# Kernel tuning notes

Measured on AMD Instinct MI355X. Metric: run time of the kernel, lower is better.

The kernel has to match this reference:

```python
import jax, jax.numpy as jnp
import numpy as np

EPS = 1e-5  # torch BatchNorm1d default

def _batchnorm(x, gamma, beta):
    # Training-mode BatchNorm1d: biased variance over the batch dim.
    mean = jnp.mean(x, axis=0)
    var = jnp.mean(jnp.square(x - mean), axis=0)
    return (x - mean) * jax.lax.rsqrt(var + EPS) * gamma + beta

def setup_inputs() -> dict:
    key = jax.random.key(0)
    ks = jax.random.split(key, 8)
    N, nfeat, nhid, nclass = 32768, 2048, 4096, 512
    x = jax.random.normal(ks[0], (N, nfeat), dtype=jnp.float32)
    y = jax.random.normal(ks[1], (N, nclass), dtype=jnp.float32)
    # Linear params (kaiming-uniform-ish scale)
    W1 = jax.random.uniform(ks[2], (nhid, nfeat), jnp.float32, -1.0, 1.0) / np.sqrt(nfeat)
    b1 = jax.random.uniform(ks[3], (nhid,), jnp.float32, -1.0, 1.0) / np.sqrt(nfeat)
    W2 = jax.random.uniform(ks[4], (nclass, nhid), jnp.float32, -1.0, 1.0) / np.sqrt(nhid)
    b2 = jax.random.uniform(ks[5], (nclass,), jnp.float32, -1.0, 1.0) / np.sqrt(nhid)
    # BatchNorm affine params (torch init: gamma=1, beta=0)
    bn1_g = jnp.ones((nfeat,), jnp.float32)
    bn1_b = jnp.zeros((nfeat,), jnp.float32)
    bn2_g = jnp.ones((nhid,), jnp.float32)
    bn2_b = jnp.zeros((nhid,), jnp.float32)
    # InteractionUnit: single learnable interaction strength beta
    beta = jnp.array(0.5, jnp.float32)
    return {"x": x, "y": y, "W1": W1, "b1": b1, "W2": W2, "b2": b2,
            "bn1_g": bn1_g, "bn1_b": bn1_b, "bn2_g": bn2_g, "bn2_b": bn2_b,
            "beta": beta}

def reference(x, y, W1, b1, W2, b2, bn1_g, bn1_b, bn2_g, bn2_b, beta):
    h = _batchnorm(x, bn1_g, bn1_b)                 # [N, nfeat]
    h = jax.nn.relu(h @ W1.T + b1)                  # [N, nhid]
    h = _batchnorm(h, bn2_g, bn2_b)                 # [N, nhid]
    out = h @ W2.T + b2 + beta * y                  # [N, nclass]
    return out
```

## Files before the change

### kernel.cpp

```cpp
#include <hip/hip_runtime.h>

typedef __bf16 v8bf __attribute__((ext_vector_type(8)));
typedef float  v16f __attribute__((ext_vector_type(16)));
typedef float  f4   __attribute__((ext_vector_type(4)));
typedef unsigned int uint;
typedef unsigned short ushort;
typedef uint   v4u  __attribute__((ext_vector_type(4)));
typedef uint   v2u  __attribute__((ext_vector_type(2)));

#define GLAS(p) ((const __attribute__((address_space(1))) void*)(p))
#define LDAS(p) ((__attribute__((address_space(3))) void*)(p))

__device__ __forceinline__ ushort f32_to_bf16(float f) {
    uint u = __builtin_bit_cast(uint, f);
    uint r = u + 0x7FFFu + ((u >> 16) & 1u);
    return (ushort)(r >> 16);
}
__device__ __forceinline__ float bflo(uint v) { return __builtin_bit_cast(float, v << 16); }
__device__ __forceinline__ float bfhi(uint v) { return __builtin_bit_cast(float, v & 0xFFFF0000u); }

__global__ void colstats_cvt(const float* __restrict__ x, ushort* __restrict__ xb,
                             float* __restrict__ sum, float* __restrict__ ssum,
                             int ncols, int rows) {
    int c4 = blockIdx.x * blockDim.x + threadIdx.x;
    int q = ncols >> 2;
    size_t base = (size_t)blockIdx.y * rows * q + c4;
    const f4* x4 = (const f4*)x;
    v2u* o = (v2u*)xb;
    f4 s = {0.f, 0.f, 0.f, 0.f}, qq = {0.f, 0.f, 0.f, 0.f};
#pragma unroll 4
    for (int r = 0; r < rows; ++r) {
        f4 v = x4[base + (size_t)r * q];
        s += v; qq += v * v;
        union { ushort us[4]; v2u u; } p;
        p.us[0] = f32_to_bf16(v.x); p.us[1] = f32_to_bf16(v.y);
        p.us[2] = f32_to_bf16(v.z); p.us[3] = f32_to_bf16(v.w);
        o[base + (size_t)r * q] = p.u;
    }
    atomicAdd(&sum[4 * c4 + 0], s.x);  atomicAdd(&ssum[4 * c4 + 0], qq.x);
    atomicAdd(&sum[4 * c4 + 1], s.y);  atomicAdd(&ssum[4 * c4 + 1], qq.y);
    atomicAdd(&sum[4 * c4 + 2], s.z);  atomicAdd(&ssum[4 * c4 + 2], qq.z);
    atomicAdd(&sum[4 * c4 + 3], s.w);  atomicAdd(&ssum[4 * c4 + 3], qq.w);
}

__global__ void colstats_bf16(const ushort* __restrict__ h, float* __restrict__ sum,
                              float* __restrict__ ssum, int ncols, int rows) {
    int cp = blockIdx.x * blockDim.x + threadIdx.x;
    int half = ncols >> 1;
    const uint* h32 = (const uint*)h;
    size_t base = (size_t)blockIdx.y * rows * half + cp;
    float s0 = 0.f, q0 = 0.f, s1 = 0.f, q1 = 0.f;
#pragma unroll 4
    for (int r = 0; r < rows; ++r) {
        uint v = h32[base + (size_t)r * half];
        float a = bflo(v), b = bfhi(v);
        s0 += a; q0 += a * a;
        s1 += b; q1 += b * b;
    }
    atomicAdd(&sum[2 * cp], s0);  atomicAdd(&ssum[2 * cp], q0);
    atomicAdd(&sum[2 * cp + 1], s1); atomicAdd(&ssum[2 * cp + 1], q1);
}

__global__ void bn_finalize(const float* __restrict__ sum, const float* __restrict__ ssum,
                            const float* __restrict__ g, const float* __restrict__ b,
                            float* __restrict__ s, float* __restrict__ t, float invN) {
    int c = blockIdx.x * blockDim.x + threadIdx.x;
    float m = sum[c] * invN;
    float var = fmaxf(ssum[c] * invN - m * m, 0.f);
    float rs = rsqrtf(var + 1e-5f);
    float sc = rs * g[c];
    s[c] = sc;
    t[c] = b[c] - m * sc;
}

__global__ void fold_w(const float* __restrict__ W, const float* __restrict__ bias,
                       const float* __restrict__ s, const float* __restrict__ t,
                       ushort* __restrict__ Wp, float* __restrict__ bp, int K) {
    int j = blockIdx.x, tx = threadIdx.x;
    const f4* row = (const f4*)(W + (size_t)j * K);
    const f4* s4 = (const f4*)s;
    const f4* t4 = (const f4*)t;
    v2u* orow = (v2u*)(Wp + (size_t)j * K);
    float part = 0.f;
    int K4 = K >> 2;
    for (int k = tx; k < K4; k += 256) {
        f4 v = row[k], sv = s4[k], tv = t4[k];
        part += v.x * tv.x + v.y * tv.y + v.z * tv.z + v.w * tv.w;
        union { ushort us[4]; v2u u; } o;
        o.us[0] = f32_to_bf16(v.x * sv.x);
        o.us[1] = f32_to_bf16(v.y * sv.y);
        o.us[2] = f32_to_bf16(v.z * sv.z);
        o.us[3] = f32_to_bf16(v.w * sv.w);
        orow[k] = o.u;
    }
    __shared__ float red[256];
    red[tx] = part;
    __syncthreads();
    for (int off = 128; off > 0; off >>= 1) {
        if (tx < off) red[tx] += red[tx + off];
        __syncthreads();
    }
    if (tx == 0) bp[j] = bias[j] + red[0];
}

template <int EPI>
__global__ __launch_bounds__(256) void gemm_bt(
    const ushort* __restrict__ A, const ushort* __restrict__ B,
    void* __restrict__ Cout, const float* __restrict__ bias,
    const float* __restrict__ Y, const float* __restrict__ betaPtr,
    int M, int Ncol, int K) {
    __shared__ __align__(16) ushort lsA[128 * 64];
    __shared__ __align__(16) ushort lsB[128 * 64];
    const int tid = threadIdx.x;
    const int wave = tid >> 6, lane = tid & 63;
    const int wm = wave >> 1, wn = wave & 1;
    const int l32 = lane & 31, lq = lane >> 5;
    const int m0 = blockIdx.y * 128, n0 = blockIdx.x * 128;

    const int srow = lane >> 3;
    const int sgc  = (lane & 7) ^ (lane >> 3);

    v16f acc[2][2] = {};

    for (int k0 = 0; k0 < K; k0 += 64) {
#pragma unroll
        for (int q = 0; q < 4; ++q) {
            const int g0 = (q * 4 + wave) << 6;
            const int row = (g0 >> 3) + srow;
            const ushort* sa = A + (size_t)(m0 + row) * K + k0 + sgc * 8;
            const ushort* sb = B + (size_t)(n0 + row) * K + k0 + sgc * 8;
            __builtin_amdgcn_global_load_lds(GLAS(sa), LDAS(&lsA[g0 * 8]), 16, 0, 0);
            __builtin_amdgcn_global_load_lds(GLAS(sb), LDAS(&lsB[g0 * 8]), 16, 0, 0);
        }
        __syncthreads();
#pragma unroll
        for (int kk = 0; kk < 64; kk += 16) {
            v8bf a[2], b[2];
            const int cbase = (kk >> 3) + lq;
#pragma unroll
            for (int i = 0; i < 2; ++i) {
                const int ra = wm * 64 + i * 32 + l32;
                const int pa = ra * 8 + (cbase ^ (ra & 7));
                a[i] = __builtin_bit_cast(v8bf, *(const v4u*)&lsA[pa * 8]);
            }
#pragma unroll
            for (int j = 0; j < 2; ++j) {
                const int rb = wn * 64 + j * 32 + l32;
                const int pb = rb * 8 + (cbase ^ (rb & 7));
                b[j] = __builtin_bit_cast(v8bf, *(const v4u*)&lsB[pb * 8]);
            }
#pragma unroll
            for (int i = 0; i < 2; ++i)
#pragma unroll
                for (int j = 0; j < 2; ++j)
                    acc[i][j] = __builtin_amdgcn_mfma_f32_32x32x16_bf16(a[i], b[j], acc[i][j], 0, 0, 0);
        }
        __syncthreads();
    }

    const float betaV = (EPI == 1) ? betaPtr[0] : 0.f;
#pragma unroll
    for (int j = 0; j < 2; ++j) {
        const int col = n0 + wn * 64 + j * 32 + l32;
        const float bj = bias[col];
#pragma unroll
        for (int i = 0; i < 2; ++i) {
#pragma unroll
            for (int reg = 0; reg < 16; ++reg) {
                const int row = m0 + wm * 64 + i * 32 + (reg & 3) + 8 * (reg >> 2) + 4 * lq;
                float v = acc[i][j][reg] + bj;
                if (EPI == 0) {
                    v = v > 0.f ? v : 0.f;
                    ((ushort*)Cout)[(size_t)row * Ncol + col] = f32_to_bf16(v);
                } else {
                    v += betaV * Y[(size_t)row * Ncol + col];
                    ((float*)Cout)[(size_t)row * Ncol + col] = v;
                }
            }
        }
    }
}

extern "C" void kernel_launch(void* const* d_in, const int* in_sizes, int n_in,
                              void* d_out, int out_size, void* d_ws, size_t ws_size,
                              hipStream_t stream) {
    const float* x    = (const float*)d_in[0];
    const float* y    = (const float*)d_in[1];
    const float* W1   = (const float*)d_in[2];
    const float* b1   = (const float*)d_in[3];
    const float* W2   = (const float*)d_in[4];
    const float* b2   = (const float*)d_in[5];
    const float* bn1g = (const float*)d_in[6];
    const float* bn1b = (const float*)d_in[7];
    const float* bn2g = (const float*)d_in[8];
    const float* bn2b = (const float*)d_in[9];
    const float* beta = (const float*)d_in[10];

    constexpr int Nb = 32768, F = 2048, H = 4096, C = 512;

    char* w = (char*)d_ws;
    ushort* xb  = (ushort*)w;
    ushort* h1  = (ushort*)(w + (size_t)Nb * F * 2);
    ushort* w1p = (ushort*)(w + (size_t)Nb * F * 2 + (size_t)Nb * H * 2);
    ushort* w2p = (ushort*)((char*)w1p + (size_t)H * F * 2);
    float*  fb  = (float*)((char*)w2p + (size_t)C * H * 2);
    float* b1p = fb;
    float* b2p = b1p + H;
    float* sum1 = b2p + C;
    float* ss1  = sum1 + F;
    float* s1   = ss1 + F;
    float* t1   = s1 + F;
    float* sum2 = t1 + F;
    float* ss2  = sum2 + H;
    float* s2   = ss2 + H;
    float* t2   = s2 + H;

    hipMemsetAsync(sum1, 0, sizeof(float) * 2 * F, stream);
    hipMemsetAsync(sum2, 0, sizeof(float) * 2 * H, stream);

    colstats_cvt<<<dim3(F / 4 / 256, 256), 256, 0, stream>>>(x, xb, sum1, ss1, F, Nb / 256);
    bn_finalize<<<F / 256, 256, 0, stream>>>(sum1, ss1, bn1g, bn1b, s1, t1, 1.f / Nb);
    fold_w<<<H, 256, 0, stream>>>(W1, b1, s1, t1, w1p, b1p, F);
    gemm_bt<0><<<dim3(H / 128, Nb / 128), 256, 0, stream>>>(xb, w1p, h1, b1p, nullptr, nullptr, Nb, H, F);
    colstats_bf16<<<dim3(H / 2 / 256, 128), 256, 0, stream>>>(h1, sum2, ss2, H, Nb / 128);
    bn_finalize<<<H / 256, 256, 0, stream>>>(sum2, ss2, bn2g, bn2b, s2, t2, 1.f / Nb);
    fold_w<<<C, 256, 0, stream>>>(W2, b2, s2, t2, w2p, b2p, H);
    gemm_bt<1><<<dim3(C / 128, Nb / 128), 256, 0, stream>>>(h1, w2p, d_out, b2p, y, beta, Nb, C, H);
    (void)in_sizes; (void)n_in; (void)out_size; (void)ws_size;
}
```

Measured before the change: 1.407 ms.

## Rewrite bf16 GEMM as 256x256 tile, 8-wave, double-buffered pipelined kernel

The GEMM goes from 128x128 tiles with 4 waves and a single LDS buffer to 256x256 tiles with 8 waves. It double-buffers LDS, staging half-tiles of the next k-slices during four compute phases, and uses explicit vmcnt/lgkmcnt waits, s_setprio and sched barriers. Workgroup IDs are remapped into an XCD-aware order for L2 locality. The aim is to raise arithmetic intensity and hide global-load latency behind MFMA work, at the cost of 128KB LDS per block, more registers and fragile hand-written wait counts.

```diff
diff --git a/kernel.cpp b/kernel.cpp
--- a/kernel.cpp
+++ b/kernel.cpp
@@ -103,72 +103,140 @@
     if (tx == 0) bp[j] = bias[j] + red[0];
 }
 
+
+__device__ __forceinline__ void stage_A(const ushort* __restrict__ Mat, ushort* dst,
+                                        int K, int k0, int ihalf, int wave, int lane) {
+    const int rs = lane >> 3;
+    const int gc = (lane & 7) ^ rs;
+    const int rb0 = ihalf * 64 + wave * 8;
+    const int rb1 = rb0 + 128;
+    const ushort* s0 = Mat + (size_t)(rb0 + rs) * K + k0 + gc * 8;
+    const ushort* s1 = Mat + (size_t)(rb1 + rs) * K + k0 + gc * 8;
+    __builtin_amdgcn_global_load_lds(GLAS(s0), LDAS(dst + rb0 * 64), 16, 0, 0);
+    __builtin_amdgcn_global_load_lds(GLAS(s1), LDAS(dst + rb1 * 64), 16, 0, 0);
+}
+__device__ __forceinline__ void stage_B(const ushort* __restrict__ Mat, ushort* dst,
+                                        int K, int k0, int jhalf, int wave, int lane) {
+    const int rs = lane >> 3;
+    const int gc = (lane & 7) ^ rs;
+    const int rb0 = (wave >> 2) * 64 + jhalf * 32 + (wave & 3) * 8;
+    const int rb1 = rb0 + 128;
+    const ushort* s0 = Mat + (size_t)(rb0 + rs) * K + k0 + gc * 8;
+    const ushort* s1 = Mat + (size_t)(rb1 + rs) * K + k0 + gc * 8;
+    __builtin_amdgcn_global_load_lds(GLAS(s0), LDAS(dst + rb0 * 64), 16, 0, 0);
+    __builtin_amdgcn_global_load_lds(GLAS(s1), LDAS(dst + rb1 * 64), 16, 0, 0);
+}
+
+#define PHASE(I, J, STAGE_STMT, WAIT_STMT)                                          \
+    {                                                                               \
+        v8bf a[2][4], b[4];                                                         \
+        _Pragma("unroll") for (int m2 = 0; m2 < 2; ++m2)                            \
+            _Pragma("unroll") for (int ks = 0; ks < 4; ++ks)                        \
+                a[m2][ks] = __builtin_bit_cast(                                     \
+                    v8bf, *(const v4u*)((const char*)curA + offA[I][m2][ks]));      \
+        _Pragma("unroll") for (int ks = 0; ks < 4; ++ks)                            \
+            b[ks] = __builtin_bit_cast(                                             \
+                v8bf, *(const v4u*)((const char*)curB + offB[J][ks]));              \
+        STAGE_STMT;                                                                 \
+        __builtin_amdgcn_s_barrier();                                               \
+        asm volatile("s_waitcnt lgkmcnt(0)" ::: "memory");                          \
+        __builtin_amdgcn_sched_barrier(0);                                          \
+        __builtin_amdgcn_s_setprio(1);                                              \
+        _Pragma("unroll") for (int ks = 0; ks < 4; ++ks)                            \
+            _Pragma("unroll") for (int m2 = 0; m2 < 2; ++m2)                        \
+                acc[I * 2 + m2][J] = __builtin_amdgcn_mfma_f32_32x32x16_bf16(       \
+                    a[m2][ks], b[ks], acc[I * 2 + m2][J], 0, 0, 0);                 \
+        __builtin_amdgcn_s_setprio(0);                                              \
+        __builtin_amdgcn_sched_barrier(0);                                          \
+        asm volatile("s_waitcnt lgkmcnt(0)" ::: "memory");                          \
+        WAIT_STMT;                                                                  \
+        __builtin_amdgcn_s_barrier();                                               \
+    }
+
 template <int EPI>
-__global__ __launch_bounds__(256) void gemm_bt(
+__global__ __launch_bounds__(512, 2) void gemm_bt(
     const ushort* __restrict__ A, const ushort* __restrict__ B,
     void* __restrict__ Cout, const float* __restrict__ bias,
     const float* __restrict__ Y, const float* __restrict__ betaPtr,
     int M, int Ncol, int K) {
-    __shared__ __align__(16) ushort lsA[128 * 64];
-    __shared__ __align__(16) ushort lsB[128 * 64];
+    __shared__ __align__(16) ushort lds[2][2][256 * 64];
     const int tid = threadIdx.x;
     const int wave = tid >> 6, lane = tid & 63;
-    const int wm = wave >> 1, wn = wave & 1;
-    const int l32 = lane & 31, lq = lane >> 5;
-    const int m0 = blockIdx.y * 128, n0 = blockIdx.x * 128;
-
-    const int srow = lane >> 3;
-    const int sgc  = (lane & 7) ^ (lane >> 3);
-
-    v16f acc[2][2] = {};
-
-    for (int k0 = 0; k0 < K; k0 += 64) {
-#pragma unroll
-        for (int q = 0; q < 4; ++q) {
-            const int g0 = (q * 4 + wave) << 6;
-            const int row = (g0 >> 3) + srow;
-            const ushort* sa = A + (size_t)(m0 + row) * K + k0 + sgc * 8;
-            const ushort* sb = B + (size_t)(n0 + row) * K + k0 + sgc * 8;
-            __builtin_amdgcn_global_load_lds(GLAS(sa), LDAS(&lsA[g0 * 8]), 16, 0, 0);
-            __builtin_amdgcn_global_load_lds(GLAS(sb), LDAS(&lsB[g0 * 8]), 16, 0, 0);
+    const int wm = wave >> 2, wn = wave & 3;
+    const int l31 = lane & 31, lq = lane >> 5;
+
+    const int gx = gridDim.x;
+    const int nwg = gx * gridDim.y;
+    int bid = blockIdx.y * gx + blockIdx.x;
+    const int qq = nwg >> 3;
+    bid = (bid & 7) * qq + (bid >> 3);
+    const int m0 = (bid / gx) * 256, n0 = (bid % gx) * 256;
+
+    const ushort* Ab = A + (size_t)m0 * K;
+    const ushort* Bb = B + (size_t)n0 * K;
+
+    int offA[2][2][4], offB[2][4];
+#pragma unroll
+    for (int I = 0; I < 2; ++I)
+#pragma unroll
+        for (int m2 = 0; m2 < 2; ++m2) {
+            const int rA = wm * 128 + I * 64 + m2 * 32 + l31;
+#pragma unroll
+            for (int ks = 0; ks < 4; ++ks)
+                offA[I][m2][ks] = (rA * 8 + ((ks * 2 + lq) ^ (rA & 7))) * 16;
         }
-        __syncthreads();
-#pragma unroll
-        for (int kk = 0; kk < 64; kk += 16) {
-            v8bf a[2], b[2];
-            const int cbase = (kk >> 3) + lq;
-#pragma unroll
-            for (int i = 0; i < 2; ++i) {
-                const int ra = wm * 64 + i * 32 + l32;
-                const int pa = ra * 8 + (cbase ^ (ra & 7));
-                a[i] = __builtin_bit_cast(v8bf, *(const v4u*)&lsA[pa * 8]);
-            }
-#pragma unroll
-            for (int j = 0; j < 2; ++j) {
-                const int rb = wn * 64 + j * 32 + l32;
-                const int pb = rb * 8 + (cbase ^ (rb & 7));
-                b[j] = __builtin_bit_cast(v8bf, *(const v4u*)&lsB[pb * 8]);
-            }
-#pragma unroll
-            for (int i = 0; i < 2; ++i)
-#pragma unroll
-                for (int j = 0; j < 2; ++j)
-                    acc[i][j] = __builtin_amdgcn_mfma_f32_32x32x16_bf16(a[i], b[j], acc[i][j], 0, 0, 0);
-        }
-        __syncthreads();
+#pragma unroll
+    for (int J = 0; J < 2; ++J) {
+        const int rB = wn * 64 + J * 32 + l31;
+#pragma unroll
+        for (int ks = 0; ks < 4; ++ks)
+            offB[J][ks] = (rB * 8 + ((ks * 2 + lq) ^ (rB & 7))) * 16;
+    }
+
+    v16f acc[4][2] = {};
+
+    const int NT = K >> 6;
+
+    stage_A(Ab, lds[0][0], K, 0, 0, wave, lane);
+    stage_B(Bb, lds[0][1], K, 0, 0, wave, lane);
+    stage_A(Ab, lds[0][0], K, 0, 1, wave, lane);
+    stage_B(Bb, lds[0][1], K, 0, 1, wave, lane);
+    if (NT > 1) {
+        stage_A(Ab, lds[1][0], K, 64, 0, wave, lane);
+        stage_B(Bb, lds[1][1], K, 64, 0, wave, lane);
+        asm volatile("s_waitcnt vmcnt(4)" ::: "memory");
+    } else {
+        asm volatile("s_waitcnt vmcnt(0)" ::: "memory");
+    }
+    __builtin_amdgcn_s_barrier();
+
+    for (int t = 0; t < NT; ++t) {
+        const int cb = t & 1, nb = cb ^ 1;
+        ushort* const curA = lds[cb][0];
+        ushort* const curB = lds[cb][1];
+        ushort* const nxtA = lds[nb][0];
+        ushort* const nxtB = lds[nb][1];
+        const int kN1 = (t + 1) << 6, kN2 = (t + 2) << 6;
+
+        PHASE(0, 0, if (t + 1 < NT) stage_A(Ab, nxtA, K, kN1, 1, wave, lane), )
+        PHASE(0, 1, if (t + 1 < NT) stage_B(Bb, nxtB, K, kN1, 1, wave, lane), )
+        PHASE(1, 0, if (t + 2 < NT) stage_A(Ab, curA, K, kN2, 0, wave, lane), )
+        PHASE(1, 1, if (t + 2 < NT) stage_B(Bb, curB, K, kN2, 0, wave, lane),
+              if (t + 2 < NT) { asm volatile("s_waitcnt vmcnt(4)" ::: "memory"); }
+              else { asm volatile("s_waitcnt vmcnt(0)" ::: "memory"); })
     }
 
     const float betaV = (EPI == 1) ? betaPtr[0] : 0.f;
 #pragma unroll
-    for (int j = 0; j < 2; ++j) {
-        const int col = n0 + wn * 64 + j * 32 + l32;
+    for (int nf = 0; nf < 2; ++nf) {
+        const int col = n0 + wn * 64 + nf * 32 + l31;
         const float bj = bias[col];
 #pragma unroll
-        for (int i = 0; i < 2; ++i) {
+        for (int mf = 0; mf < 4; ++mf) {
 #pragma unroll
             for (int reg = 0; reg < 16; ++reg) {
-                const int row = m0 + wm * 64 + i * 32 + (reg & 3) + 8 * (reg >> 2) + 4 * lq;
-                float v = acc[i][j][reg] + bj;
+                const int row = m0 + wm * 128 + mf * 32 + (reg & 3) + 8 * (reg >> 2) + 4 * lq;
+                float v = acc[mf][nf][reg] + bj;
                 if (EPI == 0) {
                     v = v > 0.f ? v : 0.f;
                     ((ushort*)Cout)[(size_t)row * Ncol + col] = f32_to_bf16(v);
@@ -179,6 +247,7 @@
             }
         }
     }
+    (void)M;
 }
 
 extern "C" void kernel_launch(void* const* d_in, const int* in_sizes, int n_in,
@@ -215,16 +284,16 @@
     float* s2   = ss2 + H;
     float* t2   = s2 + H;
 
-    hipMemsetAsync(sum1, 0, sizeof(float) * 2 * F, stream);
-    hipMemsetAsync(sum2, 0, sizeof(float) * 2 * H, stream);
+    (void)hipMemsetAsync(sum1, 0, sizeof(float) * 2 * F, stream);
+    (void)hipMemsetAsync(sum2, 0, sizeof(float) * 2 * H, stream);
 
     colstats_cvt<<<dim3(F / 4 / 256, 256), 256, 0, stream>>>(x, xb, sum1, ss1, F, Nb / 256);
     bn_finalize<<<F / 256, 256, 0, stream>>>(sum1, ss1, bn1g, bn1b, s1, t1, 1.f / Nb);
     fold_w<<<H, 256, 0, stream>>>(W1, b1, s1, t1, w1p, b1p, F);
-    gemm_bt<0><<<dim3(H / 128, Nb / 128), 256, 0, stream>>>(xb, w1p, h1, b1p, nullptr, nullptr, Nb, H, F);
+    gemm_bt<0><<<dim3(H / 256, Nb / 256), 512, 0, stream>>>(xb, w1p, h1, b1p, nullptr, nullptr, Nb, H, F);
     colstats_bf16<<<dim3(H / 2 / 256, 128), 256, 0, stream>>>(h1, sum2, ss2, H, Nb / 128);
     bn_finalize<<<H / 256, 256, 0, stream>>>(sum2, ss2, bn2g, bn2b, s2, t2, 1.f / Nb);
     fold_w<<<C, 256, 0, stream>>>(W2, b2, s2, t2, w2p, b2p, H);
-    gemm_bt<1><<<dim3(C / 128, Nb / 128), 256, 0, stream>>>(h1, w2p, d_out, b2p, y, beta, Nb, C, H);
+    gemm_bt<1><<<dim3(C / 256, Nb / 256), 512, 0, stream>>>(h1, w2p, d_out, b2p, y, beta, Nb, C, H);
     (void)in_sizes; (void)n_in; (void)out_size; (void)ws_size;
 }
```

Result: no change. 1.416 ms (+0.6%).

## Rewrite bf16 GEMM as 256x256 double-buffered pipelined kernel with 16x16 MFMA

Applied to the files above, without the earlier changes.

Replaces the 128x128 single-buffered GEMM with a 256x256-tile, 512-thread kernel. It splits each operand tile into halves held in a two-stage LDS ring and issues global-to-LDS loads for the next tiles between MFMA quadrants, using explicit vmcnt waits and barriers. It also switches to 16x16x32 MFMA with a new XOR swizzle, raises wave priority around the math, and remaps block IDs in an XCD-aware way for cache locality. The aim is to hide memory latency behind compute and improve data reuse. In exchange it needs much more LDS and registers, and the hand-managed sync makes correctness more fragile.

```diff
diff --git a/kernel.cpp b/kernel.cpp
--- a/kernel.cpp
+++ b/kernel.cpp
@@ -1,7 +1,6 @@
 #include <hip/hip_runtime.h>
 
 typedef __bf16 v8bf __attribute__((ext_vector_type(8)));
-typedef float  v16f __attribute__((ext_vector_type(16)));
 typedef float  f4   __attribute__((ext_vector_type(4)));
 typedef unsigned int uint;
 typedef unsigned short ushort;
@@ -103,72 +102,155 @@
     if (tx == 0) bp[j] = bias[j] + red[0];
 }
 
+
+__device__ __forceinline__ void stageA(const ushort* __restrict__ Mat, ushort* dstRegion,
+                                       int K, int k0, int I, int wave, int lane) {
+#pragma unroll
+    for (int h = 0; h < 2; ++h) {
+        const int rrb = h * 64 + wave * 8;
+        const int rr  = rrb + (lane >> 3);
+        const int cp  = (lane & 7) << 4;
+        const int gc  = cp ^ (((rr >> 2) & 1) << 5);
+        const int grow = (rr & 63) + ((rr >> 6) << 7) + I * 64;
+        const ushort* src = Mat + (size_t)grow * K + k0 + (gc >> 1);
+        __builtin_amdgcn_global_load_lds(GLAS(src), LDAS(dstRegion + rrb * 64), 16, 0, 0);
+    }
+}
+__device__ __forceinline__ void stageB(const ushort* __restrict__ Mat, ushort* dstRegion,
+                                       int K, int k0, int J, int wave, int lane) {
+#pragma unroll
+    for (int h = 0; h < 2; ++h) {
+        const int rrb = h * 64 + wave * 8;
+        const int rr  = rrb + (lane >> 3);
+        const int cp  = (lane & 7) << 4;
+        const int gc  = cp ^ (((rr >> 2) & 1) << 5);
+        const int gn  = (rr & 31) + ((rr >> 5) << 6) + J * 32;
+        const ushort* src = Mat + (size_t)gn * K + k0 + (gc >> 1);
+        __builtin_amdgcn_global_load_lds(GLAS(src), LDAS(dstRegion + rrb * 64), 16, 0, 0);
+    }
+}
+
+#define RD_A(rg)                                                                    \
+    _Pragma("unroll") for (int mf = 0; mf < 4; ++mf)                                \
+        _Pragma("unroll") for (int ks = 0; ks < 2; ++ks)                            \
+            a[mf][ks] = __builtin_bit_cast(                                         \
+                v8bf, *(const v4u*)((const char*)(rg) + offA[mf][ks]));
+
+#define RD_B(rg)                                                                    \
+    _Pragma("unroll") for (int nf = 0; nf < 2; ++nf)                                \
+        _Pragma("unroll") for (int ks = 0; ks < 2; ++ks)                            \
+            b[nf][ks] = __builtin_bit_cast(                                         \
+                v8bf, *(const v4u*)((const char*)(rg) + offB[nf][ks]));
+
+#define MM(I, J)                                                                    \
+    __builtin_amdgcn_s_barrier();                                                   \
+    __builtin_amdgcn_s_setprio(1);                                                  \
+    _Pragma("unroll") for (int ks = 0; ks < 2; ++ks)                                \
+        _Pragma("unroll") for (int mf = 0; mf < 4; ++mf)                            \
+            _Pragma("unroll") for (int nf = 0; nf < 2; ++nf)                        \
+                acc[(I) * 4 + mf][(J) * 2 + nf] =                                   \
+                    __builtin_amdgcn_mfma_f32_16x16x32_bf16(                        \
+                        a[mf][ks], b[nf][ks], acc[(I) * 4 + mf][(J) * 2 + nf],      \
+                        0, 0, 0);                                                   \
+    __builtin_amdgcn_s_setprio(0);
+
 template <int EPI>
-__global__ __launch_bounds__(256) void gemm_bt(
+__global__ __launch_bounds__(512, 2) void gemm_bt(
     const ushort* __restrict__ A, const ushort* __restrict__ B,
     void* __restrict__ Cout, const float* __restrict__ bias,
     const float* __restrict__ Y, const float* __restrict__ betaPtr,
     int M, int Ncol, int K) {
-    __shared__ __align__(16) ushort lsA[128 * 64];
-    __shared__ __align__(16) ushort lsB[128 * 64];
+    __shared__ __align__(16) ushort lds[2][4][128 * 64];
     const int tid = threadIdx.x;
     const int wave = tid >> 6, lane = tid & 63;
-    const int wm = wave >> 1, wn = wave & 1;
-    const int l32 = lane & 31, lq = lane >> 5;
-    const int m0 = blockIdx.y * 128, n0 = blockIdx.x * 128;
-
-    const int srow = lane >> 3;
-    const int sgc  = (lane & 7) ^ (lane >> 3);
-
-    v16f acc[2][2] = {};
-
-    for (int k0 = 0; k0 < K; k0 += 64) {
-#pragma unroll
-        for (int q = 0; q < 4; ++q) {
-            const int g0 = (q * 4 + wave) << 6;
-            const int row = (g0 >> 3) + srow;
-            const ushort* sa = A + (size_t)(m0 + row) * K + k0 + sgc * 8;
-            const ushort* sb = B + (size_t)(n0 + row) * K + k0 + sgc * 8;
-            __builtin_amdgcn_global_load_lds(GLAS(sa), LDAS(&lsA[g0 * 8]), 16, 0, 0);
-            __builtin_amdgcn_global_load_lds(GLAS(sb), LDAS(&lsB[g0 * 8]), 16, 0, 0);
-        }
-        __syncthreads();
-#pragma unroll
-        for (int kk = 0; kk < 64; kk += 16) {
-            v8bf a[2], b[2];
-            const int cbase = (kk >> 3) + lq;
-#pragma unroll
-            for (int i = 0; i < 2; ++i) {
-                const int ra = wm * 64 + i * 32 + l32;
-                const int pa = ra * 8 + (cbase ^ (ra & 7));
-                a[i] = __builtin_bit_cast(v8bf, *(const v4u*)&lsA[pa * 8]);
-            }
-#pragma unroll
-            for (int j = 0; j < 2; ++j) {
-                const int rb = wn * 64 + j * 32 + l32;
-                const int pb = rb * 8 + (cbase ^ (rb & 7));
-                b[j] = __builtin_bit_cast(v8bf, *(const v4u*)&lsB[pb * 8]);
-            }
-#pragma unroll
-            for (int i = 0; i < 2; ++i)
-#pragma unroll
-                for (int j = 0; j < 2; ++j)
-                    acc[i][j] = __builtin_amdgcn_mfma_f32_32x32x16_bf16(a[i], b[j], acc[i][j], 0, 0, 0);
-        }
-        __syncthreads();
+    const int wm = wave >> 2, wn = wave & 3;
+    const int l15 = lane & 15, l4 = lane >> 4;
+
+    const int gx = gridDim.x;
+    const int nwg = gx * gridDim.y;
+    int bid = blockIdx.y * gx + blockIdx.x;
+    const int qq = nwg >> 3;
+    bid = (bid & 7) * qq + (bid >> 3);
+    const int m0 = (bid / gx) * 256, n0 = (bid % gx) * 256;
+
+    const ushort* Ab = A + (size_t)m0 * K;
+    const ushort* Bb = B + (size_t)n0 * K;
+
+    int offA[4][2], offB[2][2];
+#pragma unroll
+    for (int mf = 0; mf < 4; ++mf) {
+        const int rr = wm * 64 + mf * 16 + l15;
+        const int sw = ((rr >> 2) & 1) << 5;
+#pragma unroll
+        for (int ks = 0; ks < 2; ++ks)
+            offA[mf][ks] = rr * 128 + ((ks * 64 + l4 * 16) ^ sw);
+    }
+#pragma unroll
+    for (int nf = 0; nf < 2; ++nf) {
+        const int rr = wn * 32 + nf * 16 + l15;
+        const int sw = ((rr >> 2) & 1) << 5;
+#pragma unroll
+        for (int ks = 0; ks < 2; ++ks)
+            offB[nf][ks] = rr * 128 + ((ks * 64 + l4 * 16) ^ sw);
+    }
+
+    f4 acc[8][4] = {};
+    v8bf a[4][2], b[2][2];
+
+    const int NT = K >> 6;
+
+    stageA(Ab, lds[0][0], K, 0, 0, wave, lane);
+    stageA(Ab, lds[0][1], K, 0, 1, wave, lane);
+    stageB(Bb, lds[0][2], K, 0, 0, wave, lane);
+    stageB(Bb, lds[0][3], K, 0, 1, wave, lane);
+    if (NT > 1) {
+        stageA(Ab, lds[1][0], K, 64, 0, wave, lane);
+        stageB(Bb, lds[1][3], K, 64, 1, wave, lane);
+        asm volatile("s_waitcnt vmcnt(4)" ::: "memory");
+    } else {
+        asm volatile("s_waitcnt vmcnt(0)" ::: "memory");
+    }
+    __builtin_amdgcn_s_barrier();
+
+    for (int t = 0; t < NT; ++t) {
+        const int cb = t & 1, nb = cb ^ 1;
+        const int kN1 = (t + 1) << 6, kN2 = (t + 2) << 6;
+
+        RD_A(lds[cb][0]);
+        RD_B(lds[cb][2]);
+        if (t + 1 < NT) stageA(Ab, lds[nb][1], K, kN1, 1, wave, lane);
+        MM(0, 0);
+        __builtin_amdgcn_s_barrier();
+
+        RD_B(lds[cb][3]);
+        if (t + 1 < NT) stageB(Bb, lds[nb][2], K, kN1, 0, wave, lane);
+        MM(0, 1);
+        __builtin_amdgcn_s_barrier();
+
+        RD_A(lds[cb][1]);
+        if (t + 2 < NT) stageA(Ab, lds[cb][0], K, kN2, 0, wave, lane);
+        MM(1, 1);
+        __builtin_amdgcn_s_barrier();
+
+        RD_B(lds[cb][2]);
+        if (t + 2 < NT) stageB(Bb, lds[cb][3], K, kN2, 1, wave, lane);
+        MM(1, 0);
+        if (t + 2 < NT) { asm volatile("s_waitcnt vmcnt(4)" ::: "memory"); }
+        else            { asm volatile("s_waitcnt vmcnt(0)" ::: "memory"); }
+        __builtin_amdgcn_s_barrier();
     }
 
     const float betaV = (EPI == 1) ? betaPtr[0] : 0.f;
 #pragma unroll
-    for (int j = 0; j < 2; ++j) {
-        const int col = n0 + wn * 64 + j * 32 + l32;
+    for (int Nf = 0; Nf < 4; ++Nf) {
+        const int col = n0 + wn * 64 + Nf * 16 + l15;
         const float bj = bias[col];
 #pragma unroll
-        for (int i = 0; i < 2; ++i) {
-#pragma unroll
-            for (int reg = 0; reg < 16; ++reg) {
-                const int row = m0 + wm * 64 + i * 32 + (reg & 3) + 8 * (reg >> 2) + 4 * lq;
-                float v = acc[i][j][reg] + bj;
+        for (int Mf = 0; Mf < 8; ++Mf) {
+#pragma unroll
+            for (int reg = 0; reg < 4; ++reg) {
+                const int row = m0 + wm * 128 + Mf * 16 + l4 * 4 + reg;
+                float v = acc[Mf][Nf][reg] + bj;
                 if (EPI == 0) {
                     v = v > 0.f ? v : 0.f;
                     ((ushort*)Cout)[(size_t)row * Ncol + col] = f32_to_bf16(v);
@@ -179,6 +261,7 @@
             }
         }
     }
+    (void)M;
 }
 
 extern "C" void kernel_launch(void* const* d_in, const int* in_sizes, int n_in,
@@ -215,16 +298,16 @@
     float* s2   = ss2 + H;
     float* t2   = s2 + H;
 
-    hipMemsetAsync(sum1, 0, sizeof(float) * 2 * F, stream);
-    hipMemsetAsync(sum2, 0, sizeof(float) * 2 * H, stream);
+    (void)hipMemsetAsync(sum1, 0, sizeof(float) * 2 * F, stream);
+    (void)hipMemsetAsync(sum2, 0, sizeof(float) * 2 * H, stream);
 
     colstats_cvt<<<dim3(F / 4 / 256, 256), 256, 0, stream>>>(x, xb, sum1, ss1, F, Nb / 256);
     bn_finalize<<<F / 256, 256, 0, stream>>>(sum1, ss1, bn1g, bn1b, s1, t1, 1.f / Nb);
     fold_w<<<H, 256, 0, stream>>>(W1, b1, s1, t1, w1p, b1p, F);
-    gemm_bt<0><<<dim3(H / 128, Nb / 128), 256, 0, stream>>>(xb, w1p, h1, b1p, nullptr, nullptr, Nb, H, F);
+    gemm_bt<0><<<dim3(H / 256, Nb / 256), 512, 0, stream>>>(xb, w1p, h1, b1p, nullptr, nullptr, Nb, H, F);
     colstats_bf16<<<dim3(H / 2 / 256, 128), 256, 0, stream>>>(h1, sum2, ss2, H, Nb / 128);
     bn_finalize<<<H / 256, 256, 0, stream>>>(sum2, ss2, bn2g, bn2b, s2, t2, 1.f / Nb);
     fold_w<<<C, 256, 0, stream>>>(W2, b2, s2, t2, w2p, b2p, H);
-    gemm_bt<1><<<dim3(C / 128, Nb / 128), 256, 0, stream>>>(h1, w2p, d_out, b2p, y, beta, Nb, C, H);
+    gemm_bt<1><<<dim3(C / 256, Nb / 256), 512, 0, stream>>>(h1, w2p, d_out, b2p, y, beta, Nb, C, H);
     (void)in_sizes; (void)n_in; (void)out_size; (void)ws_size;
 }
```

Result: faster. 1.264 ms (-10.1%).
